# Performance work log

Measured on AMD Instinct MI355X. Metric: run time of the kernel, lower is better.

## Reference

```python
import jax, jax.numpy as jnp
import numpy as np
from math import ceil

CAPACITY_FACTOR = 2.0
MIN_CAPACITY = 4


def setup_inputs() -> dict:
    key = jax.random.key(0)
    ks = jax.random.split(key, 4)
    B, S, D, Di, E = 4, 2048, 1024, 4096, 8
    x = jax.random.normal(ks[0], (B, S, D), dtype=jnp.float32)
    Wr = jax.random.normal(ks[1], (D, E), dtype=jnp.float32) * (D ** -0.5)
    W1 = jax.random.normal(ks[2], (E, D, Di), dtype=jnp.float32) * (D ** -0.5)
    b1 = jnp.zeros((E, Di), dtype=jnp.float32)
    W2 = jax.random.normal(ks[3], (E, Di, D), dtype=jnp.float32) * (Di ** -0.5)
    b2 = jnp.zeros((E, D), dtype=jnp.float32)
    return {"x": x, "Wr": Wr, "W1": W1, "b1": b1, "W2": W2, "b2": b2}


def reference(x, Wr, W1, b1, W2, b2):
    B, S, D = x.shape
    E = Wr.shape[1]
    N = B * S
    k = max(MIN_CAPACITY, ceil(N * CAPACITY_FACTOR / E))  # expert capacity (static)

    xt = x.reshape(N, D)
    scores = jax.nn.softmax(xt @ Wr, axis=-1)          # [N, E] router probs
    G, idx = jax.lax.top_k(scores.T, k)                 # [E, k]: each expert picks top-k tokens

    # dispatch: equivalent to P @ x with P = one_hot(idx, N)
    X_in = xt[idx]                                      # [E, k, D]

    # per-expert MLP (batched over experts): Linear -> GELU(exact) -> Linear
    h = jax.nn.gelu(jnp.einsum('ekd,edh->ekh', X_in, W1) + b1[:, None, :], approximate=False)
    X_e = jnp.einsum('ekh,ehd->ekd', h, W2) + b2[:, None, :]  # [E, k, D]

    # combine: einsum('ijl,ij,ijd->ld', P, G, X_e) == scatter-add of G*X_e at idx
    contrib = (G[..., None] * X_e).reshape(E * k, D)
    out = jnp.zeros((N, D), dtype=x.dtype).at[idx.reshape(-1)].add(contrib)
    return out.reshape(B, S, D)
```

## Files before the change

kernel.cpp:

```cpp
#include <hip/hip_runtime.h>
#include <hip/hip_bf16.h>
#include <cstdint>
#include <cstddef>

#define NTOK 8192
#define DMODEL 1024
#define DFF 4096
#define NEXP 8
#define CAP 2048

typedef __attribute__((ext_vector_type(8))) __bf16 bf16x8;
typedef __attribute__((ext_vector_type(4))) float f32x4;

__device__ __forceinline__ void gload16(const void* g, void* l) {
  __builtin_amdgcn_global_load_lds(
      (__attribute__((address_space(1))) void*)(g),
      (__attribute__((address_space(3))) void*)(l),
      16, 0, 0);
}
#define VMWAIT_(n) asm volatile("s_waitcnt vmcnt(" #n ")" ::: "memory")
#define VMWAIT(n) VMWAIT_(n)
#define MEMFENCE asm volatile("" ::: "memory")

__global__ __launch_bounds__(256) void zero_f32(float* p, int n4) {
  int i = blockIdx.x * blockDim.x + threadIdx.x;
  int stride = gridDim.x * blockDim.x;
  float4 z = make_float4(0.f, 0.f, 0.f, 0.f);
  for (; i < n4; i += stride) ((float4*)p)[i] = z;
}

__global__ __launch_bounds__(256) void router_kernel(
    const float* __restrict__ x, const float* __restrict__ Wr,
    float* __restrict__ scoresT, __hip_bfloat16* __restrict__ xb) {
  const int lane = threadIdx.x & 63;
  const int t = blockIdx.x * 4 + (threadIdx.x >> 6);
  const float* xr = x + (size_t)t * DMODEL;
  float acc[NEXP];
#pragma unroll
  for (int j = 0; j < NEXP; ++j) acc[j] = 0.f;
#pragma unroll
  for (int it = 0; it < DMODEL / 64; ++it) {
    int d = it * 64 + lane;
    float xv = xr[d];
    xb[(size_t)t * DMODEL + d] = __float2bfloat16(xv);
    const float4* w = (const float4*)(Wr + (size_t)d * NEXP);
    float4 w0 = w[0], w1 = w[1];
    acc[0] += xv * w0.x; acc[1] += xv * w0.y; acc[2] += xv * w0.z; acc[3] += xv * w0.w;
    acc[4] += xv * w1.x; acc[5] += xv * w1.y; acc[6] += xv * w1.z; acc[7] += xv * w1.w;
  }
#pragma unroll
  for (int off = 32; off; off >>= 1) {
#pragma unroll
    for (int j = 0; j < NEXP; ++j) acc[j] += __shfl_xor(acc[j], off);
  }
  float m = acc[0];
#pragma unroll
  for (int j = 1; j < NEXP; ++j) m = fmaxf(m, acc[j]);
  float s = 0.f;
#pragma unroll
  for (int j = 0; j < NEXP; ++j) { acc[j] = expf(acc[j] - m); s += acc[j]; }
  float inv = 1.f / s;
  if (lane < NEXP) scoresT[(size_t)lane * NTOK + t] = acc[lane] * inv;
}

__global__ __launch_bounds__(256) void topk_kernel(
    const float* __restrict__ scoresT, float* __restrict__ G, int* __restrict__ IDX) {
  __shared__ uint32_t sb[NTOK];
  __shared__ uint32_t hist[256];
  __shared__ uint32_t sfx[256];
  __shared__ uint32_t s_prefix, s_rem;
  __shared__ uint32_t eq_list[256];
  __shared__ uint32_t eq_cnt, gt_cnt;
  const int e = blockIdx.x, tid = threadIdx.x;
  const float* se = scoresT + (size_t)e * NTOK;
  for (int i = tid; i < NTOK; i += 256) sb[i] = __float_as_uint(se[i]);
  if (tid == 0) { s_prefix = 0u; s_rem = CAP; eq_cnt = 0u; gt_cnt = 0u; }
  __syncthreads();
  for (int r = 0; r < 4; ++r) {
    const int shift = 24 - 8 * r;
    hist[tid] = 0u;
    __syncthreads();
    uint32_t pfx = s_prefix;
    for (int i = tid; i < NTOK; i += 256) {
      uint32_t b = sb[i];
      if (((b >> shift) >> 8) == pfx) atomicAdd(&hist[(b >> shift) & 255u], 1u);
    }
    __syncthreads();
    sfx[tid] = hist[tid];
    __syncthreads();
#pragma unroll
    for (int off = 1; off < 256; off <<= 1) {
      uint32_t v = sfx[tid] + ((tid + off < 256) ? sfx[tid + off] : 0u);
      __syncthreads();
      sfx[tid] = v;
      __syncthreads();
    }
    uint32_t rem = s_rem;
    if (sfx[tid] >= rem && (tid == 255 || sfx[tid + 1] < rem)) {
      s_prefix = (pfx << 8) | (uint32_t)tid;
      s_rem = rem - ((tid == 255) ? 0u : sfx[tid + 1]);
    }
    __syncthreads();
  }
  const uint32_t T = s_prefix, need = s_rem;
  for (int i = tid; i < NTOK; i += 256) {
    uint32_t b = sb[i];
    if (b > T) {
      uint32_t p = atomicAdd(&gt_cnt, 1u);
      IDX[(size_t)e * CAP + p] = i;
      G[(size_t)e * CAP + p] = __uint_as_float(b);
    } else if (b == T) {
      uint32_t c = atomicAdd(&eq_cnt, 1u);
      if (c < 256u) eq_list[c] = (uint32_t)i;
    }
  }
  __syncthreads();
  if (tid == 0) {
    uint32_t base = gt_cnt;
    uint32_t c = eq_cnt < 256u ? eq_cnt : 256u;
    for (uint32_t s = 0; s < need; ++s) {
      uint32_t mv = 0xFFFFFFFFu; int mi = 0;
      for (uint32_t j = 0; j < c; ++j)
        if (eq_list[j] < mv) { mv = eq_list[j]; mi = (int)j; }
      eq_list[mi] = 0xFFFFFFFFu;
      IDX[(size_t)e * CAP + base + s] = (int)mv;
      G[(size_t)e * CAP + base + s] = __uint_as_float(T);
    }
  }
}

__global__ __launch_bounds__(256) void build_inv(
    const int* __restrict__ IDX, int* __restrict__ cnt, int* __restrict__ inv) {
  int i = blockIdx.x * 256 + threadIdx.x;
  int t = IDX[i];
  int c = atomicAdd(&cnt[t], 1);
  inv[t * 8 + c] = i;
}

__global__ __launch_bounds__(256) void combine_kernel(
    const __hip_bfloat16* __restrict__ Xe, const int* __restrict__ inv,
    const int* __restrict__ cnt, float* __restrict__ out) {
  const int w = (blockIdx.x * 256 + threadIdx.x) >> 6;
  const int lane = threadIdx.x & 63;
  const int c = cnt[w];
  float a[16];
#pragma unroll
  for (int i = 0; i < 16; ++i) a[i] = 0.f;
  for (int j = 0; j < c; ++j) {
    int s = inv[w * 8 + j];
    const bf16x8* p = (const bf16x8*)(Xe + (size_t)s * DMODEL + lane * 16);
    bf16x8 v0 = p[0], v1 = p[1];
#pragma unroll
    for (int i = 0; i < 8; ++i) {
      a[i] += (float)v0[i];
      a[8 + i] += (float)v1[i];
    }
  }
  float4* o = (float4*)(out + (size_t)w * DMODEL + lane * 16);
#pragma unroll
  for (int q = 0; q < 4; ++q)
    o[q] = make_float4(a[q * 4], a[q * 4 + 1], a[q * 4 + 2], a[q * 4 + 3]);
}

__global__ __launch_bounds__(256) void transpose_cvt(
    const float* __restrict__ in, __hip_bfloat16* __restrict__ out, int R, int C) {
  __shared__ float tile[64][68];
  const int e = blockIdx.z;
  const float* ine = in + (size_t)e * R * C;
  __hip_bfloat16* oute = out + (size_t)e * R * C;
  const int c0 = blockIdx.x * 64, r0 = blockIdx.y * 64;
  const int tid = threadIdx.x;
  const int lr = tid >> 4, lc = tid & 15;
#pragma unroll
  for (int it = 0; it < 4; ++it) {
    int row = it * 16 + lr;
    float4 v = *(const float4*)(ine + (size_t)(r0 + row) * C + c0 + lc * 4);
    *(float4*)&tile[row][lc * 4] = v;
  }
  __syncthreads();
  const int cc = tid >> 2, rq = tid & 3;
  unsigned short pk[16];
#pragma unroll
  for (int i = 0; i < 16; ++i) {
    __hip_bfloat16 b = __float2bfloat16(tile[rq * 16 + i][cc]);
    pk[i] = *(unsigned short*)&b;
  }
  char* dst = (char*)(oute + (size_t)(c0 + cc) * R + r0 + rq * 16);
  *(uint4*)dst = *(uint4*)&pk[0];
  *(uint4*)(dst + 16) = *(uint4*)&pk[8];
}

#define RD_A(BASE, H)                                                          \
  {                                                                            \
    _Pragma("unroll") for (int mi = 0; mi < 4; ++mi)                           \
        _Pragma("unroll") for (int ks = 0; ks < 2; ++ks) av[mi][ks] =          \
        *(const bf16x8*)((BASE) + Ab + offA[(H)*4 + mi][ks]);                  \
  }
#define RD_B(BASE, BV, H2)                                                     \
  {                                                                            \
    _Pragma("unroll") for (int ni = 0; ni < 2; ++ni)                           \
        _Pragma("unroll") for (int ks = 0; ks < 2; ++ks) BV[ni][ks] =          \
        *(const bf16x8*)((BASE) + Bb + offB[(H2)*2 + ni][ks]);                 \
  }
#define STAGE_A(H, BUF)                                                        \
  {                                                                            \
    gload16(pa[(H)*2], (BUF) + (H)*16384 + dst);                               \
    pa[(H)*2] += 128;                                                          \
    gload16(pa[(H)*2 + 1], (BUF) + (H)*16384 + 8192 + dst);                    \
    pa[(H)*2 + 1] += 128;                                                      \
  }
#define STAGE_B(H, BUF)                                                        \
  {                                                                            \
    gload16(pb[(H)*2], (BUF) + 32768 + (H)*16384 + dst);                       \
    pb[(H)*2] += 128;                                                          \
    gload16(pb[(H)*2 + 1], (BUF) + 32768 + (H)*16384 + 8192 + dst);            \
    pb[(H)*2 + 1] += 128;                                                      \
  }
#define PH_PRE                                                                 \
  __builtin_amdgcn_s_barrier();                                                \
  MEMFENCE;                                                                    \
  __builtin_amdgcn_s_setprio(1);
#define PH_POST __builtin_amdgcn_s_setprio(0);
#define MFMA_Q(MB, NB, BV)                                                     \
  {                                                                            \
    _Pragma("unroll") for (int mi = 0; mi < 4; ++mi)                           \
        _Pragma("unroll") for (int ni = 0; ni < 2; ++ni)                       \
            _Pragma("unroll") for (int ks = 0; ks < 2; ++ks)                   \
                acc[(MB) + mi][(NB) + ni] =                                    \
        __builtin_amdgcn_mfma_f32_16x16x32_bf16(                               \
            av[mi][ks], BV[ni][ks], acc[(MB) + mi][(NB) + ni], 0, 0, 0);       \
  }

template <int NKT>
__device__ __forceinline__ void gemm_core8(
    const char* pa0, const char* pa1, const char* pa2, const char* pa3,
    const char* pb0, const char* pb1, const char* pb2, const char* pb3,
    char* smem, f32x4 (&acc)[8][4]) {
  const int tid = threadIdx.x;
  const int wave = tid >> 6, lane = tid & 63;
  const int wm = wave >> 2, wn = wave & 3;
  const int lrow = lane & 15, lgrp = lane >> 4;
  const int dst = tid * 16;

  const char* pa[4] = {pa0, pa1, pa2, pa3};
  const char* pb[4] = {pb0, pb1, pb2, pb3};

  int offA[8][2], offB[4][2];
#pragma unroll
  for (int mi = 0; mi < 8; ++mi) {
    int rL = mi * 16 + lrow;
#pragma unroll
    for (int ks = 0; ks < 2; ++ks)
      offA[mi][ks] = rL * 128 + ((((ks * 4 + lgrp) + rL) & 7) << 4);
  }
#pragma unroll
  for (int ni = 0; ni < 4; ++ni) {
    int rL = (wn & 1) * 64 + ni * 16 + lrow;
#pragma unroll
    for (int ks = 0; ks < 2; ++ks)
      offB[ni][ks] = rL * 128 + ((((ks * 4 + lgrp) + rL) & 7) << 4);
  }
  const int Ab = wm * 16384;
  const int Bb = 32768 + (wn >> 1) * 16384;

  char* b0 = smem;
  char* b1 = smem + 65536;

#pragma unroll
  for (int g = 0; g < 4; ++g) {
    gload16(pa[g], b0 + (g >> 1) * 16384 + (g & 1) * 8192 + dst);
    pa[g] += 128;
  }
#pragma unroll
  for (int g = 0; g < 4; ++g) {
    gload16(pb[g], b0 + 32768 + (g >> 1) * 16384 + (g & 1) * 8192 + dst);
    pb[g] += 128;
  }
#pragma unroll
  for (int g = 0; g < 4; ++g) {
    gload16(pb[g], b1 + 32768 + (g >> 1) * 16384 + (g & 1) * 8192 + dst);
    pb[g] += 128;
  }
  VMWAIT(4);
  __builtin_amdgcn_s_barrier();
  MEMFENCE;

  bf16x8 av[4][2], bv0[2][2], bv1[2][2];

  for (int i = 0; i < NKT / 2; ++i) {
    const bool st2 = (2 * i + 2 < NKT);
    const bool st3 = (2 * i + 3 < NKT);

    RD_A(b0, 0); RD_B(b0, bv0, 0);
    STAGE_A(0, b1);
    PH_PRE; MFMA_Q(0, 0, bv0); PH_POST;

    RD_B(b0, bv1, 1);
    STAGE_A(1, b1);
    PH_PRE; MFMA_Q(0, 2, bv1); PH_POST;

    RD_A(b0, 1);
    if (st2) STAGE_B(0, b0);
    PH_PRE; MFMA_Q(4, 2, bv1); PH_POST;

    if (st2) STAGE_B(1, b0);
    PH_PRE; MFMA_Q(4, 0, bv0);
    __builtin_amdgcn_s_setprio(0);
    if (st2) { VMWAIT(4); } else { VMWAIT(0); }
    __builtin_amdgcn_s_barrier();
    MEMFENCE;

    RD_A(b1, 0); RD_B(b1, bv0, 0);
    if (st2) STAGE_A(0, b0);
    PH_PRE; MFMA_Q(0, 0, bv0); PH_POST;

    RD_B(b1, bv1, 1);
    if (st2) STAGE_A(1, b0);
    PH_PRE; MFMA_Q(0, 2, bv1); PH_POST;

    RD_A(b1, 1);
    if (st3) STAGE_B(0, b1);
    PH_PRE; MFMA_Q(4, 2, bv1); PH_POST;

    if (st3) STAGE_B(1, b1);
    PH_PRE; MFMA_Q(4, 0, bv0);
    __builtin_amdgcn_s_setprio(0);
    if (st3) { VMWAIT(4); }
    __builtin_amdgcn_s_barrier();
    MEMFENCE;
  }
}

__device__ __forceinline__ float gelu_tanh(float v) {
  float t = 0.7978845608028654f * (v + 0.044715f * v * v * v);
  float e = __expf(2.f * t);
  float th = 1.f - 2.f / (e + 1.f);
  return 0.5f * v * (1.f + th);
}

__global__ __launch_bounds__(512, 2) void gemm1_kernel(
    const __hip_bfloat16* __restrict__ xb,
    const __hip_bfloat16* __restrict__ W1t,
    const float* __restrict__ b1,
    const int* __restrict__ IDX,
    __hip_bfloat16* __restrict__ h, int e0, int nblk) {
  __shared__ __align__(16) char smem[131072];
  int lin = blockIdx.x;
  { int q = nblk >> 3; lin = (lin & 7) * q + (lin >> 3); }
  const int tm = lin & 7, tn = (lin >> 3) & 15, ez = lin >> 7;
  const int e = e0 + ez;
  const int tid = threadIdx.x, wave = tid >> 6, lane = tid & 63;
  const int wm = wave >> 2, wn = wave & 3;
  const int lrow = lane & 15, lgrp = lane >> 4;

  const int r0 = tid >> 3;
  const int ksrc = (((tid & 7) - r0) & 7) * 16;
  const char* pa[4]; const char* pb[4];
#pragma unroll
  for (int g = 0; g < 4; ++g) {
    int m = g * 64 + r0;
    int tok = IDX[e * CAP + tm * 256 + m];
    pa[g] = (const char*)(xb + (size_t)tok * DMODEL) + ksrc;
    int n = g * 64 + r0;
    pb[g] = (const char*)(W1t + ((size_t)e * DFF + tn * 256 + n) * DMODEL) + ksrc;
  }

  f32x4 acc[8][4];
  f32x4 zero = {0.f, 0.f, 0.f, 0.f};
#pragma unroll
  for (int mi = 0; mi < 8; ++mi)
#pragma unroll
    for (int ni = 0; ni < 4; ++ni) acc[mi][ni] = zero;

  gemm_core8<DMODEL / 64>(pa[0], pa[1], pa[2], pa[3],
                          pb[0], pb[1], pb[2], pb[3], smem, acc);

  __hip_bfloat16* he = h + (size_t)ez * CAP * DFF;
  const float* b1e = b1 + (size_t)e * DFF;
  float bvals[4];
#pragma unroll
  for (int ni = 0; ni < 4; ++ni)
    bvals[ni] = b1e[tn * 256 + wn * 64 + ni * 16 + lrow];
  char* sb = smem;
  const int wswz = lgrp << 5;
#pragma unroll
  for (int mi = 0; mi < 8; ++mi) {
#pragma unroll
    for (int j = 0; j < 4; ++j) {
      int row = wm * 128 + mi * 16 + lgrp * 4 + j;
#pragma unroll
      for (int ni = 0; ni < 4; ++ni) {
        int col = wn * 64 + ni * 16 + lrow;
        float v = acc[mi][ni][j] + bvals[ni];
        v = gelu_tanh(v);
        *(__hip_bfloat16*)(sb + ((row * 512 + col * 2) ^ wswz)) =
            __float2bfloat16(v);
      }
    }
  }
  __syncthreads();
  size_t obase = (size_t)(tm * 256) * DFF + tn * 256;
#pragma unroll
  for (int c = 0; c < 16; ++c) {
    int byte = c * 8192 + tid * 16;
    int row = byte >> 9;
    int rswz = ((row >> 2) & 3) << 5;
    bf16x8 vals = *(const bf16x8*)(sb + (byte ^ rswz));
    int col = (byte & 511) >> 1;
    *(bf16x8*)(he + obase + (size_t)row * DFF + col) = vals;
  }
}

__global__ __launch_bounds__(512, 2) void gemm2_kernel(
    const __hip_bfloat16* __restrict__ h,
    const __hip_bfloat16* __restrict__ W2t,
    const float* __restrict__ b2,
    const float* __restrict__ G,
    __hip_bfloat16* __restrict__ Xe, int e0, int nblk) {
  __shared__ __align__(16) char smem[131072];
  int lin = blockIdx.x;
  { int q = nblk >> 3; lin = (lin & 7) * q + (lin >> 3); }
  const int tm = lin & 7, tn = (lin >> 3) & 3, ez = lin >> 5;
  const int e = e0 + ez;
  const int tid = threadIdx.x, wave = tid >> 6, lane = tid & 63;
  const int wm = wave >> 2, wn = wave & 3;
  const int lrow = lane & 15, lgrp = lane >> 4;

  const int r0 = tid >> 3;
  const int ksrc = (((tid & 7) - r0) & 7) * 16;
  const char* pa[4]; const char* pb[4];
#pragma unroll
  for (int g = 0; g < 4; ++g) {
    int m = g * 64 + r0;
    pa[g] = (const char*)(h + ((size_t)ez * CAP + tm * 256 + m) * DFF) + ksrc;
    int n = g * 64 + r0;
    pb[g] = (const char*)(W2t + ((size_t)e * DMODEL + tn * 256 + n) * DFF) + ksrc;
  }

  f32x4 acc[8][4];
  f32x4 zero = {0.f, 0.f, 0.f, 0.f};
#pragma unroll
  for (int mi = 0; mi < 8; ++mi)
#pragma unroll
    for (int ni = 0; ni < 4; ++ni) acc[mi][ni] = zero;

  gemm_core8<DFF / 64>(pa[0], pa[1], pa[2], pa[3],
                       pb[0], pb[1], pb[2], pb[3], smem, acc);

  const float* b2e = b2 + (size_t)e * DMODEL;
  const float* ge = G + (size_t)e * CAP + tm * 256;
  float bvals[4];
#pragma unroll
  for (int ni = 0; ni < 4; ++ni)
    bvals[ni] = b2e[tn * 256 + wn * 64 + ni * 16 + lrow];
  char* sb = smem;
  const int wswz = lgrp << 5;
#pragma unroll
  for (int mi = 0; mi < 8; ++mi) {
#pragma unroll
    for (int j = 0; j < 4; ++j) {
      int row = wm * 128 + mi * 16 + lgrp * 4 + j;
      float g = ge[row];
#pragma unroll
      for (int ni = 0; ni < 4; ++ni) {
        int col = wn * 64 + ni * 16 + lrow;
        float v = (acc[mi][ni][j] + bvals[ni]) * g;
        *(__hip_bfloat16*)(sb + ((row * 512 + col * 2) ^ wswz)) =
            __float2bfloat16(v);
      }
    }
  }
  __syncthreads();
  __hip_bfloat16* xbase = Xe + ((size_t)(e * CAP + tm * 256)) * DMODEL + tn * 256;
#pragma unroll
  for (int c = 0; c < 16; ++c) {
    int byte = c * 8192 + tid * 16;
    int row = byte >> 9;
    int rswz = ((row >> 2) & 3) << 5;
    bf16x8 vals = *(const bf16x8*)(sb + (byte ^ rswz));
    int col = (byte & 511) >> 1;
    *(bf16x8*)(xbase + (size_t)row * DMODEL + col) = vals;
  }
}

extern "C" void kernel_launch(void* const* d_in, const int* in_sizes, int n_in,
                              void* d_out, int out_size, void* d_ws, size_t ws_size,
                              hipStream_t stream) {
  const float* x  = (const float*)d_in[0];
  const float* Wr = (const float*)d_in[1];
  const float* W1 = (const float*)d_in[2];
  const float* b1 = (const float*)d_in[3];
  const float* W2 = (const float*)d_in[4];
  const float* b2 = (const float*)d_in[5];
  float* out = (float*)d_out;
  char* ws = (char*)d_ws;

  size_t off = 0;
  float* scoresT = (float*)(ws + off); off += (size_t)NEXP * NTOK * 4;
  float* G       = (float*)(ws + off); off += (size_t)NEXP * CAP * 4;
  int*   IDX     = (int*)(ws + off);   off += (size_t)NEXP * CAP * 4;
  int*   cnt     = (int*)(ws + off);   off += (size_t)NTOK * 4;
  int*   inv     = (int*)(ws + off);   off += (size_t)NTOK * 8 * 4;
  __hip_bfloat16* xb  = (__hip_bfloat16*)(ws + off); off += (size_t)NTOK * DMODEL * 2;
  __hip_bfloat16* W1t = (__hip_bfloat16*)(ws + off); off += (size_t)NEXP * DFF * DMODEL * 2;
  __hip_bfloat16* W2t = (__hip_bfloat16*)(ws + off); off += (size_t)NEXP * DMODEL * DFF * 2;
  __hip_bfloat16* Xe  = (__hip_bfloat16*)(ws + off); off += (size_t)NEXP * CAP * DMODEL * 2;
  __hip_bfloat16* hbuf = (__hip_bfloat16*)(ws + off);
  size_t h_per_e = (size_t)CAP * DFF * 2;
  size_t avail = (ws_size > off) ? (ws_size - off) : 0;
  int EC = (int)(avail / h_per_e);
  if (EC < 1) EC = 1;
  if (EC > NEXP) EC = NEXP;

  zero_f32<<<8, 256, 0, stream>>>((float*)cnt, NTOK / 4);
  router_kernel<<<NTOK / 4, 256, 0, stream>>>(x, Wr, scoresT, xb);
  topk_kernel<<<NEXP, 256, 0, stream>>>(scoresT, G, IDX);
  build_inv<<<NEXP * CAP / 256, 256, 0, stream>>>(IDX, cnt, inv);
  transpose_cvt<<<dim3(DFF / 64, DMODEL / 64, NEXP), 256, 0, stream>>>(
      W1, W1t, DMODEL, DFF);
  transpose_cvt<<<dim3(DMODEL / 64, DFF / 64, NEXP), 256, 0, stream>>>(
      W2, W2t, DFF, DMODEL);
  for (int e0 = 0; e0 < NEXP; e0 += EC) {
    int ne = (NEXP - e0 < EC) ? (NEXP - e0) : EC;
    int nblk1 = 128 * ne;
    gemm1_kernel<<<nblk1, 512, 0, stream>>>(xb, W1t, b1, IDX, hbuf, e0, nblk1);
    int nblk2 = 32 * ne;
    gemm2_kernel<<<nblk2, 512, 0, stream>>>(hbuf, W2t, b2, G, Xe, e0, nblk2);
  }
  combine_kernel<<<NTOK / 4, 256, 0, stream>>>(Xe, inv, cnt, out);
}
```

Before: 412.9 us.

## Fuse small prep kernels and interleave expert blocks in GEMM grid mapping

Moves the zeroing of the per-token counter into the router kernel and builds the inverse token-to-slot map inside topk, so the separate zero and build_inv launches go away. The two weight transpose launches become a single kernel that picks W1 or W2 from its flat block index. The GEMM block mapping changes so that consecutive blocks cycle across experts instead of the earlier grouped swizzle, which shifts how work and cache locality are spread over CUs. This trims launch overhead but makes topk issue global atomics from only 8 blocks, and the new GEMM ordering may lower L2 reuse of shared weight tiles.

Result: no change. 412.2 us, median of 2 (-0.2%).

```diff
diff --git a/kernel.cpp b/kernel.cpp
--- a/kernel.cpp
+++ b/kernel.cpp
@@ -22,18 +22,13 @@
 #define VMWAIT(n) VMWAIT_(n)
 #define MEMFENCE asm volatile("" ::: "memory")
 
-__global__ __launch_bounds__(256) void zero_f32(float* p, int n4) {
-  int i = blockIdx.x * blockDim.x + threadIdx.x;
-  int stride = gridDim.x * blockDim.x;
-  float4 z = make_float4(0.f, 0.f, 0.f, 0.f);
-  for (; i < n4; i += stride) ((float4*)p)[i] = z;
-}
-
 __global__ __launch_bounds__(256) void router_kernel(
     const float* __restrict__ x, const float* __restrict__ Wr,
-    float* __restrict__ scoresT, __hip_bfloat16* __restrict__ xb) {
+    float* __restrict__ scoresT, __hip_bfloat16* __restrict__ xb,
+    int* __restrict__ cnt) {
   const int lane = threadIdx.x & 63;
   const int t = blockIdx.x * 4 + (threadIdx.x >> 6);
+  if (lane == 0) cnt[t] = 0;
   const float* xr = x + (size_t)t * DMODEL;
   float acc[NEXP];
 #pragma unroll
@@ -64,7 +59,8 @@
 }
 
 __global__ __launch_bounds__(256) void topk_kernel(
-    const float* __restrict__ scoresT, float* __restrict__ G, int* __restrict__ IDX) {
+    const float* __restrict__ scoresT, float* __restrict__ G,
+    int* __restrict__ IDX, int* __restrict__ cnt, int* __restrict__ inv) {
   __shared__ uint32_t sb[NTOK];
   __shared__ uint32_t hist[256];
   __shared__ uint32_t sfx[256];
@@ -107,8 +103,11 @@
     uint32_t b = sb[i];
     if (b > T) {
       uint32_t p = atomicAdd(&gt_cnt, 1u);
-      IDX[(size_t)e * CAP + p] = i;
-      G[(size_t)e * CAP + p] = __uint_as_float(b);
+      int slot = e * CAP + (int)p;
+      IDX[slot] = i;
+      G[slot] = __uint_as_float(b);
+      int c = atomicAdd(&cnt[i], 1);
+      inv[i * 8 + c] = slot;
     } else if (b == T) {
       uint32_t c = atomicAdd(&eq_cnt, 1u);
       if (c < 256u) eq_list[c] = (uint32_t)i;
@@ -123,18 +122,13 @@
       for (uint32_t j = 0; j < c; ++j)
         if (eq_list[j] < mv) { mv = eq_list[j]; mi = (int)j; }
       eq_list[mi] = 0xFFFFFFFFu;
-      IDX[(size_t)e * CAP + base + s] = (int)mv;
-      G[(size_t)e * CAP + base + s] = __uint_as_float(T);
-    }
-  }
-}
-
-__global__ __launch_bounds__(256) void build_inv(
-    const int* __restrict__ IDX, int* __restrict__ cnt, int* __restrict__ inv) {
-  int i = blockIdx.x * 256 + threadIdx.x;
-  int t = IDX[i];
-  int c = atomicAdd(&cnt[t], 1);
-  inv[t * 8 + c] = i;
+      int slot = e * CAP + (int)(base + s);
+      IDX[slot] = (int)mv;
+      G[slot] = __uint_as_float(T);
+      int cc = atomicAdd(&cnt[mv], 1);
+      inv[mv * 8 + cc] = slot;
+    }
+  }
 }
 
 __global__ __launch_bounds__(256) void combine_kernel(
@@ -162,13 +156,23 @@
     o[q] = make_float4(a[q * 4], a[q * 4 + 1], a[q * 4 + 2], a[q * 4 + 3]);
 }
 
-__global__ __launch_bounds__(256) void transpose_cvt(
-    const float* __restrict__ in, __hip_bfloat16* __restrict__ out, int R, int C) {
+__global__ __launch_bounds__(256) void transpose_cvt2(
+    const float* __restrict__ W1, __hip_bfloat16* __restrict__ W1t,
+    const float* __restrict__ W2, __hip_bfloat16* __restrict__ W2t) {
   __shared__ float tile[64][68];
-  const int e = blockIdx.z;
+  int b = blockIdx.x;
+  const float* in; __hip_bfloat16* out; int R, C, bx, by, e;
+  if (b < 8192) {
+    in = W1; out = W1t; R = DMODEL; C = DFF;
+    e = b >> 10; int t = b & 1023; bx = t & 63; by = t >> 6;
+  } else {
+    b -= 8192;
+    in = W2; out = W2t; R = DFF; C = DMODEL;
+    e = b >> 10; int t = b & 1023; bx = t & 15; by = t >> 4;
+  }
   const float* ine = in + (size_t)e * R * C;
   __hip_bfloat16* oute = out + (size_t)e * R * C;
-  const int c0 = blockIdx.x * 64, r0 = blockIdx.y * 64;
+  const int c0 = bx * 64, r0 = by * 64;
   const int tid = threadIdx.x;
   const int lr = tid >> 4, lc = tid & 15;
 #pragma unroll
@@ -182,8 +186,8 @@
   unsigned short pk[16];
 #pragma unroll
   for (int i = 0; i < 16; ++i) {
-    __hip_bfloat16 b = __float2bfloat16(tile[rq * 16 + i][cc]);
-    pk[i] = *(unsigned short*)&b;
+    __hip_bfloat16 bb = __float2bfloat16(tile[rq * 16 + i][cc]);
+    pk[i] = *(unsigned short*)&bb;
   }
   char* dst = (char*)(oute + (size_t)(c0 + cc) * R + r0 + rq * 16);
   *(uint4*)dst = *(uint4*)&pk[0];
@@ -343,11 +347,12 @@
     const __hip_bfloat16* __restrict__ W1t,
     const float* __restrict__ b1,
     const int* __restrict__ IDX,
-    __hip_bfloat16* __restrict__ h, int e0, int nblk) {
+    __hip_bfloat16* __restrict__ h, int e0, int ne) {
   __shared__ __align__(16) char smem[131072];
-  int lin = blockIdx.x;
-  { int q = nblk >> 3; lin = (lin & 7) * q + (lin >> 3); }
-  const int tm = lin & 7, tn = (lin >> 3) & 15, ez = lin >> 7;
+  int s = blockIdx.x;
+  const int ez = s % ne;
+  int r = s / ne;
+  const int tm = r & 7, tn = r >> 3;
   const int e = e0 + ez;
   const int tid = threadIdx.x, wave = tid >> 6, lane = tid & 63;
   const int wm = wave >> 2, wn = wave & 3;
@@ -416,11 +421,12 @@
     const __hip_bfloat16* __restrict__ W2t,
     const float* __restrict__ b2,
     const float* __restrict__ G,
-    __hip_bfloat16* __restrict__ Xe, int e0, int nblk) {
+    __hip_bfloat16* __restrict__ Xe, int e0, int ne) {
   __shared__ __align__(16) char smem[131072];
-  int lin = blockIdx.x;
-  { int q = nblk >> 3; lin = (lin & 7) * q + (lin >> 3); }
-  const int tm = lin & 7, tn = (lin >> 3) & 3, ez = lin >> 5;
+  int s = blockIdx.x;
+  const int ez = s % ne;
+  int r = s / ne;
+  const int tm = r & 7, tn = r >> 3;
   const int e = e0 + ez;
   const int tid = threadIdx.x, wave = tid >> 6, lane = tid & 63;
   const int wm = wave >> 2, wn = wave & 3;
@@ -512,20 +518,13 @@
   if (EC < 1) EC = 1;
   if (EC > NEXP) EC = NEXP;
 
-  zero_f32<<<8, 256, 0, stream>>>((float*)cnt, NTOK / 4);
-  router_kernel<<<NTOK / 4, 256, 0, stream>>>(x, Wr, scoresT, xb);
-  topk_kernel<<<NEXP, 256, 0, stream>>>(scoresT, G, IDX);
-  build_inv<<<NEXP * CAP / 256, 256, 0, stream>>>(IDX, cnt, inv);
-  transpose_cvt<<<dim3(DFF / 64, DMODEL / 64, NEXP), 256, 0, stream>>>(
-      W1, W1t, DMODEL, DFF);
-  transpose_cvt<<<dim3(DMODEL / 64, DFF / 64, NEXP), 256, 0, stream>>>(
-      W2, W2t, DFF, DMODEL);
+  router_kernel<<<NTOK / 4, 256, 0, stream>>>(x, Wr, scoresT, xb, cnt);
+  topk_kernel<<<NEXP, 256, 0, stream>>>(scoresT, G, IDX, cnt, inv);
+  transpose_cvt2<<<16384, 256, 0, stream>>>(W1, W1t, W2, W2t);
   for (int e0 = 0; e0 < NEXP; e0 += EC) {
     int ne = (NEXP - e0 < EC) ? (NEXP - e0) : EC;
-    int nblk1 = 128 * ne;
-    gemm1_kernel<<<nblk1, 512, 0, stream>>>(xb, W1t, b1, IDX, hbuf, e0, nblk1);
-    int nblk2 = 32 * ne;
-    gemm2_kernel<<<nblk2, 512, 0, stream>>>(hbuf, W2t, b2, G, Xe, e0, nblk2);
+    gemm1_kernel<<<128 * ne, 512, 0, stream>>>(xb, W1t, b1, IDX, hbuf, e0, ne);
+    gemm2_kernel<<<32 * ne, 512, 0, stream>>>(hbuf, W2t, b2, G, Xe, e0, ne);
   }
   combine_kernel<<<NTOK / 4, 256, 0, stream>>>(Xe, inv, cnt, out);
 }
```
